# Performance work log

Measured on AMD Instinct MI355X. Metric: run time of the kernel, lower is better.

The kernel has to match this reference:

```python
import math
import jax, jax.numpy as jnp
import numpy as np

B, T, IN, D, H, L = 128, 1024, 32, 128, 8, 2
U = max(1, min(int(5 * math.log(T + 1)), T))  # ProbSparse sampled queries = 34


def setup_inputs() -> dict:
    key = jax.random.key(0)
    ks = jax.random.split(key, 12)
    def w(k, shape):
        fan_in = shape[-2]
        return jax.random.normal(k, shape, jnp.float32) / jnp.sqrt(jnp.float32(fan_in))
    idx = jnp.stack([jax.random.permutation(jax.random.fold_in(ks[1], l), T)[:U]
                     for l in range(L)]).astype(jnp.int64 if jax.config.jax_enable_x64 else jnp.int32)
    return {
        "x": jax.random.normal(ks[0], (B, T, IN), jnp.float32),
        "idx": idx,
        "proj_w": w(ks[2], (IN, D)), "proj_b": jnp.zeros((D,), jnp.float32),
        "wq": w(ks[3], (L, D, D)), "wk": w(ks[4], (L, D, D)), "wv": w(ks[5], (L, D, D)),
        "wo": w(ks[6], (L, D, D)), "wo_b": jnp.zeros((L, D), jnp.float32),
        "ln1_g": jnp.ones((L, D), jnp.float32), "ln1_b": jnp.zeros((L, D), jnp.float32),
        "ff1_w": w(ks[7], (L, D, 4 * D)), "ff1_b": jnp.zeros((L, 4 * D), jnp.float32),
        "ff2_w": w(ks[8], (L, 4 * D, D)), "ff2_b": jnp.zeros((L, D), jnp.float32),
        "ln2_g": jnp.ones((L, D), jnp.float32), "ln2_b": jnp.zeros((L, D), jnp.float32),
        "head_g": jnp.ones((D,), jnp.float32), "head_bb": jnp.zeros((D,), jnp.float32),
        "head_w": w(ks[9], (D, 1)), "head_wb": jnp.zeros((1,), jnp.float32),
    }


def _ln(x, g, b, eps=1e-5):
    m = x.mean(-1, keepdims=True)
    v = ((x - m) ** 2).mean(-1, keepdims=True)
    return (x - m) / jnp.sqrt(v + eps) * g + b


def _pos_encoding():
    pos = jnp.arange(T, dtype=jnp.float32)[:, None]
    div = jnp.exp(jnp.arange(0, D, 2, dtype=jnp.float32) * (-math.log(10000.0) / D))
    # interleave sin/cos -> [T, D]
    return jnp.stack([jnp.sin(pos * div), jnp.cos(pos * div)], axis=-1).reshape(T, D)


def reference(x, idx, proj_w, proj_b, wq, wk, wv, wo, wo_b, ln1_g, ln1_b,
              ff1_w, ff1_b, ff2_w, ff2_b, ln2_g, ln2_b,
              head_g, head_bb, head_w, head_wb):
    Dh = D // H
    h = x @ proj_w + proj_b + _pos_encoding()[None]  # [B,T,D]
    for l in range(L):
        q = (h @ wq[l]).reshape(B, T, H, Dh).transpose(0, 2, 1, 3)
        k = (h @ wk[l]).reshape(B, T, H, Dh).transpose(0, 2, 1, 3)
        v = (h @ wv[l]).reshape(B, T, H, Dh).transpose(0, 2, 1, 3)
        qs = q[:, :, idx[l], :]  # gather sampled queries [B,H,U,Dh]
        scores = jnp.einsum('bhud,bhtd->bhut', qs, k) / jnp.sqrt(jnp.float32(Dh))
        attn = jax.nn.softmax(scores, axis=-1)
        ctx = jnp.einsum('bhut,bhtd->bhud', attn, v)  # [B,H,U,Dh]
        base = jnp.broadcast_to(ctx.mean(axis=2, keepdims=True), (B, H, T, Dh))
        out = base.at[:, :, idx[l], :].set(ctx)  # scatter back
        attn_out = out.transpose(0, 2, 1, 3).reshape(B, T, D) @ wo[l] + wo_b[l]
        h = _ln(h + attn_out, ln1_g[l], ln1_b[l])
        ff = jax.nn.gelu(h @ ff1_w[l] + ff1_b[l], approximate=False) @ ff2_w[l] + ff2_b[l]
        h = _ln(h + ff, ln2_g[l], ln2_b[l])
    last = _ln(h[:, -1, :], head_g, head_bb)
    return (last @ head_w + head_wb).squeeze(-1)  # [B]
```

## Files before the change

kernel.cpp:

```cpp
#include <hip/hip_runtime.h>
#include <math.h>

constexpr int B  = 128;
constexpr int T  = 1024;
constexpr int IN_DIM = 32;
constexpr int D  = 128;
constexpr int H  = 8;
constexpr int DH = 16;
constexpr int L  = 2;
constexpr int U  = 34;
constexpr int FF = 512;

typedef __attribute__((ext_vector_type(8))) _Float16 f16x8;
typedef __attribute__((ext_vector_type(2))) _Float16 h2;
typedef __attribute__((ext_vector_type(4))) float f32x4;

__device__ __forceinline__ unsigned short f2h(float x) {
  union { _Float16 h; unsigned short u; } v;
  v.h = (_Float16)x;
  return v.u;
}

__device__ __forceinline__ h2 shfl_xor_h2(h2 v, int off) {
  union { h2 h; int i; } u;
  u.h = v;
  u.i = __shfl_xor(u.i, off);
  return u.h;
}

__device__ __forceinline__ float erf_fast(float x) {
  float a = fabsf(x);
  float t = __builtin_amdgcn_rcpf(fmaf(0.3275911f, a, 1.f));
  float y = t * (0.254829592f +
            t * (-0.284496736f +
            t * (1.421413741f +
            t * (-1.453152027f +
            t * 1.061405429f))));
  float r = 1.f - y * __expf(-a * a);
  return copysignf(r, x);
}


__device__ __forceinline__ void blockMax2(float& a, float& b, float* red) {
  for (int off = 32; off; off >>= 1) {
    a = fmaxf(a, __shfl_down(a, off));
    b = fmaxf(b, __shfl_down(b, off));
  }
  if ((threadIdx.x & 63) == 0) {
    red[threadIdx.x >> 6] = a;
    red[4 + (threadIdx.x >> 6)] = b;
  }
  __syncthreads();
  a = fmaxf(fmaxf(red[0], red[1]), fmaxf(red[2], red[3]));
  b = fmaxf(fmaxf(red[4], red[5]), fmaxf(red[6], red[7]));
  __syncthreads();
}

__device__ __forceinline__ void blockSum2(float& a, float& b, float* red) {
  for (int off = 32; off; off >>= 1) {
    a += __shfl_down(a, off);
    b += __shfl_down(b, off);
  }
  if ((threadIdx.x & 63) == 0) {
    red[threadIdx.x >> 6] = a;
    red[4 + (threadIdx.x >> 6)] = b;
  }
  __syncthreads();
  a = red[0] + red[1] + red[2] + red[3];
  b = red[4] + red[5] + red[6] + red[7];
  __syncthreads();
}


__global__ void k_prep_all(const float* __restrict__ wk_l,
                           const float* __restrict__ wv_l,
                           const float* __restrict__ w1_l,
                           const float* __restrict__ w2_l,
                           unsigned short* __restrict__ wkT,
                           unsigned short* __restrict__ wvT,
                           unsigned short* __restrict__ w1T,
                           unsigned short* __restrict__ w2T) {
  int idx = blockIdx.x * 256 + threadIdx.x;
  if (idx < 16384) {
    int n = idx >> 7, k = idx & 127;
    wkT[idx] = f2h(wk_l[k * 128 + n]);
  } else if (idx < 32768) {
    int j = idx - 16384;
    int n = j >> 7, k = j & 127;
    wvT[j] = f2h(wv_l[k * 128 + n]);
  } else if (idx < 98304) {
    int j = idx - 32768;
    int n = j >> 7, k = j & 127;
    w1T[j] = f2h(w1_l[k * 512 + n]);
  } else if (idx < 163840) {
    int j = idx - 98304;
    int n = j >> 9, k = j & 511;
    w2T[j] = f2h(w2_l[k * 128 + n]);
  }
}

__global__ __launch_bounds__(D) void k_proj(const float* __restrict__ x,
                                            const float* __restrict__ pw,
                                            const float* __restrict__ pb,
                                            float* __restrict__ h) {
  int row = blockIdx.x;
  int t = row & (T - 1);
  int d = threadIdx.x;
  __shared__ float xs[IN_DIM];
  if (threadIdx.x < IN_DIM) xs[threadIdx.x] = x[(size_t)row * IN_DIM + threadIdx.x];
  __syncthreads();
  float acc = pb[d];
#pragma unroll
  for (int i = 0; i < IN_DIM; ++i) acc += xs[i] * pw[i * D + d];
  int j = d >> 1;
  float div = __expf((float)(2 * j) * (-logf(10000.f) / (float)D));
  float ang = (float)t * div;
  acc += (d & 1) ? __cosf(ang) : __sinf(ang);
  h[(size_t)row * D + d] = acc;
}

__global__ __launch_bounds__(256) void k_kv_mfma2(
    const float* __restrict__ h,
    const unsigned short* __restrict__ wkt,
    const unsigned short* __restrict__ wvt,
    unsigned short* __restrict__ kbuf, unsigned short* __restrict__ vbuf) {
  __shared__ unsigned short hsb[16 * 128];
  const int tid = threadIdx.x;
  const int r0 = blockIdx.x * 16;
  {
    int m = tid >> 4, kc = tid & 15;
    const float* src = h + (size_t)(r0 + m) * D + kc * 8;
    float4 x0 = *(const float4*)src;
    float4 x1 = *(const float4*)(src + 4);
    f16x8 p;
    p[0] = (_Float16)x0.x; p[1] = (_Float16)x0.y;
    p[2] = (_Float16)x0.z; p[3] = (_Float16)x0.w;
    p[4] = (_Float16)x1.x; p[5] = (_Float16)x1.y;
    p[6] = (_Float16)x1.z; p[7] = (_Float16)x1.w;
    int byte = (m << 8) + (kc << 4);
    byte ^= (m & 7) << 4;
    *(f16x8*)((char*)hsb + byte) = p;
  }
  __syncthreads();
  const int wv = tid >> 6;
  const int l15 = tid & 15;
  const int lq = (tid & 63) >> 4;
  f16x8 afr[4];
#pragma unroll
  for (int ks = 0; ks < 4; ++ks) {
    int byte = (l15 << 8) + ks * 64 + (lq << 4);
    byte ^= (l15 & 7) << 4;
    afr[ks] = *(const f16x8*)((const char*)hsb + byte);
  }
  const unsigned short* wt = (wv < 2) ? wkt : wvt;
  unsigned short* outp = (wv < 2) ? kbuf : vbuf;
  const int cw = (wv & 1) * 64;
  f32x4 acc[4];
#pragma unroll
  for (int nt = 0; nt < 4; ++nt) acc[nt] = (f32x4){0.f, 0.f, 0.f, 0.f};
#pragma unroll
  for (int nt = 0; nt < 4; ++nt) {
    const unsigned short* wp = wt + (size_t)(cw + nt * 16 + l15) * 128 + lq * 8;
#pragma unroll
    for (int ks = 0; ks < 4; ++ks) {
      f16x8 bf = *(const f16x8*)(wp + ks * 32);
      acc[nt] = __builtin_amdgcn_mfma_f32_16x16x32_f16(afr[ks], bf, acc[nt], 0, 0, 0);
    }
  }
#pragma unroll
  for (int nt = 0; nt < 4; ++nt) {
    int col = cw + nt * 16 + l15;
    int hcol = col >> 4, dh = col & 15;
#pragma unroll
    for (int r = 0; r < 4; ++r) {
      int row = r0 + 4 * lq + r;
      int b = row >> 10, t = row & (T - 1);
      outp[(((size_t)b * H + hcol) * T + t) * DH + dh] = f2h(acc[nt][r]);
    }
  }
}

__global__ __launch_bounds__(D) void k_qrow(const float* __restrict__ h,
                                            const int* __restrict__ idx,
                                            const float* __restrict__ wq,
                                            float* __restrict__ qs) {
  int bu = blockIdx.x;
  int b = bu / U, u = bu - b * U;
  int t = idx[u];
  __shared__ float hs[D];
  hs[threadIdx.x] = h[((size_t)b * T + t) * D + threadIdx.x];
  __syncthreads();
  int d = threadIdx.x;
  float acc = 0.f;
  for (int k = 0; k < D; ++k) acc += hs[k] * wq[k * D + d];
  qs[(size_t)bu * D + d] = acc;
}

__global__ __launch_bounds__(256) void k_attn6(const float* __restrict__ qs,
                                               const unsigned short* __restrict__ kbuf,
                                               const unsigned short* __restrict__ vbuf,
                                               float* __restrict__ ctx) {
  constexpr int NWG = B * H * 17;
  int bid = blockIdx.x;
  int orig = (bid & 7) * (NWG / 8) + (bid >> 3);
  int up = orig % 17;
  int gb = orig / 17;
  int hh = gb & 7, b = gb >> 3;
  int u0 = up * 2;

  __shared__ float sc[2][T];
  __shared__ h2 qh[2][8];
  __shared__ float red[8];
  __shared__ float redw[4][2][DH];
  const int tid = threadIdx.x;

  if (tid < 16) {
    int uu = tid >> 3, jj = tid & 7;
    const float* qp = qs + ((size_t)b * U + u0 + uu) * D + hh * DH + jj * 2;
    qh[uu][jj] = (h2){(_Float16)qp[0], (_Float16)qp[1]};
  }
  __syncthreads();
  const unsigned short* kg = kbuf + (size_t)gb * T * DH;
  const unsigned short* vg = vbuf + (size_t)gb * T * DH;

  h2 q0[8], q1[8];
#pragma unroll
  for (int j = 0; j < 8; ++j) { q0[j] = qh[0][j]; q1[j] = qh[1][j]; }

  float lmax0 = -1e30f, lmax1 = -1e30f;
  for (int t = tid; t < T; t += 256) {
    const h2* k2 = (const h2*)(kg + t * DH);
    float s0 = 0.f, s1 = 0.f;
#pragma unroll
    for (int j = 0; j < 8; ++j) {
      h2 kv = k2[j];
      s0 = __builtin_amdgcn_fdot2(q0[j], kv, s0, false);
      s1 = __builtin_amdgcn_fdot2(q1[j], kv, s1, false);
    }
    s0 *= 0.25f; s1 *= 0.25f;
    sc[0][t] = s0; sc[1][t] = s1;
    lmax0 = fmaxf(lmax0, s0);
    lmax1 = fmaxf(lmax1, s1);
  }
  blockMax2(lmax0, lmax1, red);
  float lsum0 = 0.f, lsum1 = 0.f;
  for (int t = tid; t < T; t += 256) {
    float e0 = __expf(sc[0][t] - lmax0);
    float e1 = __expf(sc[1][t] - lmax1);
    sc[0][t] = e0; sc[1][t] = e1;
    lsum0 += e0; lsum1 += e1;
  }
  blockSum2(lsum0, lsum1, red);
  float inv0 = 1.f / lsum0;
  float inv1 = 1.f / lsum1;

  h2 p0[8], p1[8];
#pragma unroll
  for (int j = 0; j < 8; ++j) { p0[j] = (h2){0, 0}; p1[j] = (h2){0, 0}; }
  for (int t = tid; t < T; t += 256) {
    const h2* v2 = (const h2*)(vg + t * DH);
    _Float16 a0 = (_Float16)sc[0][t], a1 = (_Float16)sc[1][t];
    h2 a0h = (h2){a0, a0}, a1h = (h2){a1, a1};
#pragma unroll
    for (int j = 0; j < 8; ++j) {
      h2 vv = v2[j];
      p0[j] += a0h * vv;
      p1[j] += a1h * vv;
    }
  }
#pragma unroll
  for (int j = 0; j < 8; ++j) {
#pragma unroll
    for (int off = 32; off; off >>= 1) {
      p0[j] += shfl_xor_h2(p0[j], off);
      p1[j] += shfl_xor_h2(p1[j], off);
    }
  }
  const int wv = tid >> 6, lane = tid & 63;
  if (lane == 0) {
#pragma unroll
    for (int j = 0; j < 8; ++j) {
      redw[wv][0][2 * j]     = (float)p0[j][0];
      redw[wv][0][2 * j + 1] = (float)p0[j][1];
      redw[wv][1][2 * j]     = (float)p1[j][0];
      redw[wv][1][2 * j + 1] = (float)p1[j][1];
    }
  }
  __syncthreads();
  if (tid < 32) {
    int uu = tid >> 4, dh = tid & 15;
    float tot = redw[0][uu][dh] + redw[1][uu][dh] + redw[2][uu][dh] + redw[3][uu][dh];
    float inv = uu ? inv1 : inv0;
    ctx[((size_t)b * U + u0 + uu) * D + hh * DH + dh] = tot * inv;
  }
}

__global__ __launch_bounds__(D) void k_bc(const float* __restrict__ ctx,
                                          const float* __restrict__ wo,
                                          const float* __restrict__ wob,
                                          float* __restrict__ ctxo,
                                          float* __restrict__ baseo) {
  int i = blockIdx.x;
  int b = i / (U + 1), u = i - b * (U + 1);
  int d = threadIdx.x;
  __shared__ float cs[D];
  if (u < U) {
    cs[d] = ctx[((size_t)b * U + u) * D + d];
  } else {
    float s = 0.f;
    for (int uu = 0; uu < U; ++uu) s += ctx[((size_t)b * U + uu) * D + d];
    cs[d] = s * (1.f / (float)U);
  }
  __syncthreads();
  float acc = wob[d];
  for (int k = 0; k < D; ++k) acc += cs[k] * wo[k * D + d];
  if (u < U) ctxo[((size_t)b * U + u) * D + d] = acc;
  else       baseo[(size_t)b * D + d] = acc;
}

__global__ void k_map(const int* __restrict__ idx, int* __restrict__ map) {
  int t = blockIdx.x * 256 + threadIdx.x;
  if (t >= T) return;
  int m = -1;
  for (int u = 0; u < U; ++u)
    if (idx[u] == t) m = u;
  map[t] = m;
}

constexpr int RF2 = 32;
constexpr int YSS = 129;
__global__ __launch_bounds__(512) void k_ff5b(
    const float* __restrict__ h,
    const float* __restrict__ ctxo,
    const float* __restrict__ baseo,
    const int* __restrict__ map,
    const float* __restrict__ g1,
    const float* __restrict__ b1n,
    const unsigned short* __restrict__ w1t,
    const float* __restrict__ b1,
    const unsigned short* __restrict__ w2t,
    const float* __restrict__ b2,
    const float* __restrict__ g2,
    const float* __restrict__ bb2,
    float* __restrict__ hout) {
  __shared__ unsigned short hsb[RF2 * 128];
  __shared__ unsigned short g16[RF2][520];

  const int tid = threadIdx.x;
  const int r0 = blockIdx.x * RF2;

  {
    int m = tid >> 4, kc = tid & 15;
    int row = r0 + m;
    int b = row >> 10, t = row & (T - 1);
    int u = map[t];
    const float* src = (u >= 0) ? ctxo + ((size_t)b * U + u) * D
                                : baseo + (size_t)b * D;
    const float* hp = h + (size_t)row * D + kc * 8;
    float4 x0 = *(const float4*)hp;
    float4 x1 = *(const float4*)(hp + 4);
    float4 a0 = *(const float4*)(src + kc * 8);
    float4 a1 = *(const float4*)(src + kc * 8 + 4);
    float y0 = x0.x + a0.x, y1 = x0.y + a0.y, y2 = x0.z + a0.z, y3 = x0.w + a0.w;
    float y4 = x1.x + a1.x, y5 = x1.y + a1.y, y6 = x1.z + a1.z, y7 = x1.w + a1.w;
    float s = y0 + y1 + y2 + y3 + y4 + y5 + y6 + y7;
#pragma unroll
    for (int off = 8; off; off >>= 1) s += __shfl_xor(s, off, 16);
    float mu = s * (1.f / D);
    float e0 = y0 - mu, e1 = y1 - mu, e2 = y2 - mu, e3 = y3 - mu;
    float e4 = y4 - mu, e5 = y5 - mu, e6 = y6 - mu, e7 = y7 - mu;
    float v2 = e0 * e0 + e1 * e1 + e2 * e2 + e3 * e3 +
               e4 * e4 + e5 * e5 + e6 * e6 + e7 * e7;
#pragma unroll
    for (int off = 8; off; off >>= 1) v2 += __shfl_xor(v2, off, 16);
    float inv = rsqrtf(v2 * (1.f / D) + 1e-5f);
    float4 gv0 = *(const float4*)(g1 + kc * 8);
    float4 gv1 = *(const float4*)(g1 + kc * 8 + 4);
    float4 bv0 = *(const float4*)(b1n + kc * 8);
    float4 bv1 = *(const float4*)(b1n + kc * 8 + 4);
    f16x8 p;
    p[0] = (_Float16)(e0 * inv * gv0.x + bv0.x);
    p[1] = (_Float16)(e1 * inv * gv0.y + bv0.y);
    p[2] = (_Float16)(e2 * inv * gv0.z + bv0.z);
    p[3] = (_Float16)(e3 * inv * gv0.w + bv0.w);
    p[4] = (_Float16)(e4 * inv * gv1.x + bv1.x);
    p[5] = (_Float16)(e5 * inv * gv1.y + bv1.y);
    p[6] = (_Float16)(e6 * inv * gv1.z + bv1.z);
    p[7] = (_Float16)(e7 * inv * gv1.w + bv1.w);
    int byte = (m << 8) + (kc << 4);
    byte ^= (m & 7) << 4;
    *(f16x8*)((char*)hsb + byte) = p;
  }
  __syncthreads();

  const int wv = tid >> 6;
  const int l15 = tid & 15;
  const int lq = (tid & 63) >> 4;

  f16x8 afr[2][4];
#pragma unroll
  for (int mt = 0; mt < 2; ++mt)
#pragma unroll
    for (int ks = 0; ks < 4; ++ks) {
      int m = mt * 16 + l15;
      int byte = (m << 8) + ks * 64 + (lq << 4);
      byte ^= (m & 7) << 4;
      afr[mt][ks] = *(const f16x8*)((const char*)hsb + byte);
    }

  for (int nt = 0; nt < 4; ++nt) {
    int n0 = wv * 64 + nt * 16;
    const unsigned short* wp = w1t + (size_t)(n0 + l15) * 128 + lq * 8;
    f32x4 a0 = (f32x4){0.f, 0.f, 0.f, 0.f};
    f32x4 a1 = (f32x4){0.f, 0.f, 0.f, 0.f};
#pragma unroll
    for (int ks = 0; ks < 4; ++ks) {
      f16x8 bf = *(const f16x8*)(wp + ks * 32);
      a0 = __builtin_amdgcn_mfma_f32_16x16x32_f16(afr[0][ks], bf, a0, 0, 0, 0);
      a1 = __builtin_amdgcn_mfma_f32_16x16x32_f16(afr[1][ks], bf, a1, 0, 0, 0);
    }
    float bcol = b1[n0 + l15];
#pragma unroll
    for (int r = 0; r < 4; ++r) {
      int row0 = 4 * lq + r;
      float v0 = a0[r] + bcol;
      v0 = 0.5f * v0 * (1.f + erf_fast(v0 * 0.70710678118654752f));
      g16[row0][n0 + l15] = f2h(v0);
      float v1 = a1[r] + bcol;
      v1 = 0.5f * v1 * (1.f + erf_fast(v1 * 0.70710678118654752f));
      g16[row0 + 16][n0 + l15] = f2h(v1);
    }
  }
  __syncthreads();

  f32x4 a2a[2], a2b[2];
  a2a[0] = (f32x4){0.f, 0.f, 0.f, 0.f};
  a2a[1] = (f32x4){0.f, 0.f, 0.f, 0.f};
  a2b[0] = (f32x4){0.f, 0.f, 0.f, 0.f};
  a2b[1] = (f32x4){0.f, 0.f, 0.f, 0.f};
  const int ncol = wv * 16 + l15;
  const unsigned short* wp2b = w2t + (size_t)ncol * 512;
  for (int ks = 0; ks < 8; ++ks) {
    int k0 = ks * 32 + lq * 8;
    int k1 = (ks + 8) * 32 + lq * 8;
    f16x8 x0 = *(const f16x8*)&g16[l15][k0];
    f16x8 x1 = *(const f16x8*)&g16[16 + l15][k0];
    f16x8 w0 = *(const f16x8*)(wp2b + k0);
    a2a[0] = __builtin_amdgcn_mfma_f32_16x16x32_f16(x0, w0, a2a[0], 0, 0, 0);
    a2a[1] = __builtin_amdgcn_mfma_f32_16x16x32_f16(x1, w0, a2a[1], 0, 0, 0);
    f16x8 y0 = *(const f16x8*)&g16[l15][k1];
    f16x8 y1 = *(const f16x8*)&g16[16 + l15][k1];
    f16x8 w1 = *(const f16x8*)(wp2b + k1);
    a2b[0] = __builtin_amdgcn_mfma_f32_16x16x32_f16(y0, w1, a2b[0], 0, 0, 0);
    a2b[1] = __builtin_amdgcn_mfma_f32_16x16x32_f16(y1, w1, a2b[1], 0, 0, 0);
  }
  f32x4 acc2[2];
#pragma unroll
  for (int mt = 0; mt < 2; ++mt) {
    acc2[mt][0] = a2a[mt][0] + a2b[mt][0];
    acc2[mt][1] = a2a[mt][1] + a2b[mt][1];
    acc2[mt][2] = a2a[mt][2] + a2b[mt][2];
    acc2[mt][3] = a2a[mt][3] + a2b[mt][3];
  }
  __syncthreads();

  float* ys = (float*)&g16[0][0];
  {
    float bc = b2[ncol];
#pragma unroll
    for (int mt = 0; mt < 2; ++mt)
#pragma unroll
      for (int r = 0; r < 4; ++r) {
        int row = mt * 16 + 4 * lq + r;
        int byte = (row << 8) + ((ncol * 2) ^ ((row & 7) << 4));
        float h1 = (float)(*(const _Float16*)((const char*)hsb + byte));
        ys[row * YSS + ncol] = h1 + acc2[mt][r] + bc;
      }
  }
  __syncthreads();

  {
    int row = tid >> 4, lane16 = tid & 15;
    const float* yr = ys + row * YSS;
    float yv[8];
    float s = 0.f;
#pragma unroll
    for (int j = 0; j < 8; ++j) {
      yv[j] = yr[lane16 + j * 16];
      s += yv[j];
    }
#pragma unroll
    for (int off = 8; off; off >>= 1) s += __shfl_xor(s, off, 16);
    float mu = s * (1.f / D);
    float v2 = 0.f;
#pragma unroll
    for (int j = 0; j < 8; ++j) {
      float e = yv[j] - mu;
      v2 += e * e;
    }
#pragma unroll
    for (int off = 8; off; off >>= 1) v2 += __shfl_xor(v2, off, 16);
    float inv = rsqrtf(v2 * (1.f / D) + 1e-5f);
    float* op = hout + (size_t)(r0 + row) * D;
#pragma unroll
    for (int j = 0; j < 8; ++j) {
      int dd = lane16 + j * 16;
      op[dd] = (yv[j] - mu) * inv * g2[dd] + bb2[dd];
    }
  }
}

__global__ __launch_bounds__(D) void k_head(const float* __restrict__ h,
                                            const float* __restrict__ g,
                                            const float* __restrict__ bb,
                                            const float* __restrict__ hw,
                                            const float* __restrict__ hwb,
                                            float* __restrict__ out) {
  int b = blockIdx.x, d = threadIdx.x;
  float y = h[((size_t)b * T + (T - 1)) * D + d];
  __shared__ float red[2];
  float s = y;
  for (int off = 32; off; off >>= 1) s += __shfl_down(s, off);
  if ((threadIdx.x & 63) == 0) red[threadIdx.x >> 6] = s;
  __syncthreads();
  float m = (red[0] + red[1]) * (1.f / D);
  __syncthreads();
  float e = y - m;
  float v = e * e;
  for (int off = 32; off; off >>= 1) v += __shfl_down(v, off);
  if ((threadIdx.x & 63) == 0) red[threadIdx.x >> 6] = v;
  __syncthreads();
  float inv = rsqrtf((red[0] + red[1]) * (1.f / D) + 1e-5f);
  __syncthreads();
  float last = e * inv * g[d] + bb[d];
  float p = last * hw[d];
  for (int off = 32; off; off >>= 1) p += __shfl_down(p, off);
  if ((threadIdx.x & 63) == 0) red[threadIdx.x >> 6] = p;
  __syncthreads();
  if (threadIdx.x == 0) out[b] = red[0] + red[1] + hwb[0];
}


extern "C" void kernel_launch(void* const* d_in, const int* in_sizes, int n_in,
                              void* d_out, int out_size, void* d_ws, size_t ws_size,
                              hipStream_t stream) {
  const float* x       = (const float*)d_in[0];
  const int*   idx     = (const int*)d_in[1];
  const float* proj_w  = (const float*)d_in[2];
  const float* proj_b  = (const float*)d_in[3];
  const float* wq      = (const float*)d_in[4];
  const float* wk      = (const float*)d_in[5];
  const float* wv      = (const float*)d_in[6];
  const float* wo      = (const float*)d_in[7];
  const float* wo_b    = (const float*)d_in[8];
  const float* ln1_g   = (const float*)d_in[9];
  const float* ln1_b   = (const float*)d_in[10];
  const float* ff1_w   = (const float*)d_in[11];
  const float* ff1_b   = (const float*)d_in[12];
  const float* ff2_w   = (const float*)d_in[13];
  const float* ff2_b   = (const float*)d_in[14];
  const float* ln2_g   = (const float*)d_in[15];
  const float* ln2_b   = (const float*)d_in[16];
  const float* head_g  = (const float*)d_in[17];
  const float* head_bb = (const float*)d_in[18];
  const float* head_w  = (const float*)d_in[19];
  const float* head_wb = (const float*)d_in[20];
  float* out = (float*)d_out;

  float* wsf  = (float*)d_ws;
  float* h    = wsf;
  float* kreg = h    + (size_t)B * T * D;
  float* vreg = kreg + (size_t)B * T * D;
  float* qs   = vreg + (size_t)B * T * D;
  float* ctx  = qs   + (size_t)B * U * D;
  float* ctxo = ctx  + (size_t)B * U * D;
  float* baseo= ctxo + (size_t)B * U * D;
  int*   map  = (int*)(baseo + (size_t)B * D);
  unsigned short* kbuf16 = (unsigned short*)kreg;
  unsigned short* vbuf16 = (unsigned short*)vreg;
  unsigned short* wbuf = (unsigned short*)(map + 1024);
  const size_t PL = 16384 + 16384 + 65536 + 65536;

  for (int l = 0; l < L; ++l) {
    unsigned short* wkT = wbuf + (size_t)l * PL;
    unsigned short* wvT = wkT + 16384;
    unsigned short* w1T = wvT + 16384;
    unsigned short* w2T = w1T + 65536;
    k_prep_all<<<640, 256, 0, stream>>>(wk + (size_t)l * D * D,
                                        wv + (size_t)l * D * D,
                                        ff1_w + (size_t)l * D * FF,
                                        ff2_w + (size_t)l * FF * D,
                                        wkT, wvT, w1T, w2T);
  }

  k_proj<<<B * T, D, 0, stream>>>(x, proj_w, proj_b, h);

  for (int l = 0; l < L; ++l) {
    const float* wq_l = wq + (size_t)l * D * D;
    const float* wo_l = wo + (size_t)l * D * D;
    const int*   idx_l = idx + l * U;
    unsigned short* wkT = wbuf + (size_t)l * PL;
    unsigned short* wvT = wkT + 16384;
    unsigned short* w1T = wvT + 16384;
    unsigned short* w2T = w1T + 65536;

    k_kv_mfma2<<<B * T / 16, 256, 0, stream>>>(h, wkT, wvT, kbuf16, vbuf16);
    k_qrow<<<B * U, D, 0, stream>>>(h, idx_l, wq_l, qs);
    k_attn6<<<B * H * 17, 256, 0, stream>>>(qs, kbuf16, vbuf16, ctx);
    k_bc<<<B * (U + 1), D, 0, stream>>>(ctx, wo_l, wo_b + l * D, ctxo, baseo);
    k_map<<<(T + 255) / 256, 256, 0, stream>>>(idx_l, map);
    k_ff5b<<<B * T / RF2, 512, 0, stream>>>(h, ctxo, baseo, map,
                                            ln1_g + l * D, ln1_b + l * D,
                                            w1T, ff1_b + l * FF,
                                            w2T, ff2_b + l * D,
                                            ln2_g + l * D, ln2_b + l * D, h);
  }

  k_head<<<B, D, 0, stream>>>(h, head_g, head_bb, head_w, head_wb, out);
}
```

Baseline: 765.3 us.

## Restructure FFN kernel so each wave owns 16 rows with streamed FF chunks

The fused LN1+FFN+LN2 kernel is reorganised so each wave independently processes 16 rows. The 512-wide hidden dimension is streamed in 32-column chunks: each chunk's GELU output goes to a tiny per-wave LDS buffer and is immediately consumed by the second GEMM, with accumulators held in registers. All block-level __syncthreads are removed and LN2 is done with in-register shuffles. The intent is to cut block synchronisation and LDS round-trips. In exchange each wave now streams all of W1 and W2 from global/L2 for only 16 rows, so per-row weight traffic goes up, and register pressure rises.

```diff
diff --git a/kernel.cpp b/kernel.cpp
--- a/kernel.cpp
+++ b/kernel.cpp
@@ -327,9 +327,7 @@
   map[t] = m;
 }
 
-constexpr int RF2 = 32;
-constexpr int YSS = 129;
-__global__ __launch_bounds__(512) void k_ff5b(
+__global__ __launch_bounds__(512) void k_ff7(
     const float* __restrict__ h,
     const float* __restrict__ ctxo,
     const float* __restrict__ baseo,
@@ -343,169 +341,155 @@
     const float* __restrict__ g2,
     const float* __restrict__ bb2,
     float* __restrict__ hout) {
-  __shared__ unsigned short hsb[RF2 * 128];
-  __shared__ unsigned short g16[RF2][520];
+  __shared__ __align__(16) char smem[8 * 4096 + 8 * 1280];
 
   const int tid = threadIdx.x;
-  const int r0 = blockIdx.x * RF2;
+  const int w = tid >> 6;
+  const int lane = tid & 63;
+  const int l15 = lane & 15;
+  const int lq = lane >> 4;
+  const int r0 = blockIdx.x * 128 + w * 16;
+  char* h1w = smem + w * 4096;
+  char* gp  = smem + 8 * 4096 + w * 1280;
 
   {
-    int m = tid >> 4, kc = tid & 15;
-    int row = r0 + m;
-    int b = row >> 10, t = row & (T - 1);
-    int u = map[t];
-    const float* src = (u >= 0) ? ctxo + ((size_t)b * U + u) * D
-                                : baseo + (size_t)b * D;
-    const float* hp = h + (size_t)row * D + kc * 8;
-    float4 x0 = *(const float4*)hp;
-    float4 x1 = *(const float4*)(hp + 4);
-    float4 a0 = *(const float4*)(src + kc * 8);
-    float4 a1 = *(const float4*)(src + kc * 8 + 4);
-    float y0 = x0.x + a0.x, y1 = x0.y + a0.y, y2 = x0.z + a0.z, y3 = x0.w + a0.w;
-    float y4 = x1.x + a1.x, y5 = x1.y + a1.y, y6 = x1.z + a1.z, y7 = x1.w + a1.w;
-    float s = y0 + y1 + y2 + y3 + y4 + y5 + y6 + y7;
-#pragma unroll
-    for (int off = 8; off; off >>= 1) s += __shfl_xor(s, off, 16);
-    float mu = s * (1.f / D);
-    float e0 = y0 - mu, e1 = y1 - mu, e2 = y2 - mu, e3 = y3 - mu;
-    float e4 = y4 - mu, e5 = y5 - mu, e6 = y6 - mu, e7 = y7 - mu;
-    float v2 = e0 * e0 + e1 * e1 + e2 * e2 + e3 * e3 +
-               e4 * e4 + e5 * e5 + e6 * e6 + e7 * e7;
-#pragma unroll
-    for (int off = 8; off; off >>= 1) v2 += __shfl_xor(v2, off, 16);
-    float inv = rsqrtf(v2 * (1.f / D) + 1e-5f);
-    float4 gv0 = *(const float4*)(g1 + kc * 8);
-    float4 gv1 = *(const float4*)(g1 + kc * 8 + 4);
-    float4 bv0 = *(const float4*)(b1n + kc * 8);
-    float4 bv1 = *(const float4*)(b1n + kc * 8 + 4);
-    f16x8 p;
-    p[0] = (_Float16)(e0 * inv * gv0.x + bv0.x);
-    p[1] = (_Float16)(e1 * inv * gv0.y + bv0.y);
-    p[2] = (_Float16)(e2 * inv * gv0.z + bv0.z);
-    p[3] = (_Float16)(e3 * inv * gv0.w + bv0.w);
-    p[4] = (_Float16)(e4 * inv * gv1.x + bv1.x);
-    p[5] = (_Float16)(e5 * inv * gv1.y + bv1.y);
-    p[6] = (_Float16)(e6 * inv * gv1.z + bv1.z);
-    p[7] = (_Float16)(e7 * inv * gv1.w + bv1.w);
-    int byte = (m << 8) + (kc << 4);
-    byte ^= (m & 7) << 4;
-    *(f16x8*)((char*)hsb + byte) = p;
-  }
-  __syncthreads();
-
-  const int wv = tid >> 6;
-  const int l15 = tid & 15;
-  const int lq = (tid & 63) >> 4;
-
-  f16x8 afr[2][4];
-#pragma unroll
-  for (int mt = 0; mt < 2; ++mt)
-#pragma unroll
-    for (int ks = 0; ks < 4; ++ks) {
-      int m = mt * 16 + l15;
-      int byte = (m << 8) + ks * 64 + (lq << 4);
-      byte ^= (m & 7) << 4;
-      afr[mt][ks] = *(const f16x8*)((const char*)hsb + byte);
-    }
-
-  for (int nt = 0; nt < 4; ++nt) {
-    int n0 = wv * 64 + nt * 16;
-    const unsigned short* wp = w1t + (size_t)(n0 + l15) * 128 + lq * 8;
-    f32x4 a0 = (f32x4){0.f, 0.f, 0.f, 0.f};
-    f32x4 a1 = (f32x4){0.f, 0.f, 0.f, 0.f};
-#pragma unroll
-    for (int ks = 0; ks < 4; ++ks) {
-      f16x8 bf = *(const f16x8*)(wp + ks * 32);
-      a0 = __builtin_amdgcn_mfma_f32_16x16x32_f16(afr[0][ks], bf, a0, 0, 0, 0);
-      a1 = __builtin_amdgcn_mfma_f32_16x16x32_f16(afr[1][ks], bf, a1, 0, 0, 0);
-    }
-    float bcol = b1[n0 + l15];
-#pragma unroll
-    for (int r = 0; r < 4; ++r) {
-      int row0 = 4 * lq + r;
-      float v0 = a0[r] + bcol;
-      v0 = 0.5f * v0 * (1.f + erf_fast(v0 * 0.70710678118654752f));
-      g16[row0][n0 + l15] = f2h(v0);
-      float v1 = a1[r] + bcol;
-      v1 = 0.5f * v1 * (1.f + erf_fast(v1 * 0.70710678118654752f));
-      g16[row0 + 16][n0 + l15] = f2h(v1);
-    }
-  }
-  __syncthreads();
-
-  f32x4 a2a[2], a2b[2];
-  a2a[0] = (f32x4){0.f, 0.f, 0.f, 0.f};
-  a2a[1] = (f32x4){0.f, 0.f, 0.f, 0.f};
-  a2b[0] = (f32x4){0.f, 0.f, 0.f, 0.f};
-  a2b[1] = (f32x4){0.f, 0.f, 0.f, 0.f};
-  const int ncol = wv * 16 + l15;
-  const unsigned short* wp2b = w2t + (size_t)ncol * 512;
-  for (int ks = 0; ks < 8; ++ks) {
-    int k0 = ks * 32 + lq * 8;
-    int k1 = (ks + 8) * 32 + lq * 8;
-    f16x8 x0 = *(const f16x8*)&g16[l15][k0];
-    f16x8 x1 = *(const f16x8*)&g16[16 + l15][k0];
-    f16x8 w0 = *(const f16x8*)(wp2b + k0);
-    a2a[0] = __builtin_amdgcn_mfma_f32_16x16x32_f16(x0, w0, a2a[0], 0, 0, 0);
-    a2a[1] = __builtin_amdgcn_mfma_f32_16x16x32_f16(x1, w0, a2a[1], 0, 0, 0);
-    f16x8 y0 = *(const f16x8*)&g16[l15][k1];
-    f16x8 y1 = *(const f16x8*)&g16[16 + l15][k1];
-    f16x8 w1 = *(const f16x8*)(wp2b + k1);
-    a2b[0] = __builtin_amdgcn_mfma_f32_16x16x32_f16(y0, w1, a2b[0], 0, 0, 0);
-    a2b[1] = __builtin_amdgcn_mfma_f32_16x16x32_f16(y1, w1, a2b[1], 0, 0, 0);
-  }
-  f32x4 acc2[2];
-#pragma unroll
-  for (int mt = 0; mt < 2; ++mt) {
-    acc2[mt][0] = a2a[mt][0] + a2b[mt][0];
-    acc2[mt][1] = a2a[mt][1] + a2b[mt][1];
-    acc2[mt][2] = a2a[mt][2] + a2b[mt][2];
-    acc2[mt][3] = a2a[mt][3] + a2b[mt][3];
-  }
-  __syncthreads();
-
-  float* ys = (float*)&g16[0][0];
-  {
-    float bc = b2[ncol];
-#pragma unroll
-    for (int mt = 0; mt < 2; ++mt)
-#pragma unroll
-      for (int r = 0; r < 4; ++r) {
-        int row = mt * 16 + 4 * lq + r;
-        int byte = (row << 8) + ((ncol * 2) ^ ((row & 7) << 4));
-        float h1 = (float)(*(const _Float16*)((const char*)hsb + byte));
-        ys[row * YSS + ncol] = h1 + acc2[mt][r] + bc;
-      }
-  }
-  __syncthreads();
-
-  {
-    int row = tid >> 4, lane16 = tid & 15;
-    const float* yr = ys + row * YSS;
-    float yv[8];
+    int row = r0 + l15;
+    int bb = row >> 10, tt = row & (T - 1);
+    int u = map[tt];
+    const float* src = (u >= 0) ? ctxo + ((size_t)bb * U + u) * D
+                                : baseo + (size_t)bb * D;
+    const float* hp = h + (size_t)row * D + lq * 32;
+    const float* ap = src + lq * 32;
+    float y[32];
     float s = 0.f;
 #pragma unroll
     for (int j = 0; j < 8; ++j) {
-      yv[j] = yr[lane16 + j * 16];
-      s += yv[j];
-    }
-#pragma unroll
-    for (int off = 8; off; off >>= 1) s += __shfl_xor(s, off, 16);
+      float4 hv = *(const float4*)(hp + j * 4);
+      float4 av = *(const float4*)(ap + j * 4);
+      y[j * 4 + 0] = hv.x + av.x;
+      y[j * 4 + 1] = hv.y + av.y;
+      y[j * 4 + 2] = hv.z + av.z;
+      y[j * 4 + 3] = hv.w + av.w;
+      s += y[j * 4 + 0] + y[j * 4 + 1] + y[j * 4 + 2] + y[j * 4 + 3];
+    }
+    s += __shfl_xor(s, 16);
+    s += __shfl_xor(s, 32);
     float mu = s * (1.f / D);
     float v2 = 0.f;
 #pragma unroll
-    for (int j = 0; j < 8; ++j) {
-      float e = yv[j] - mu;
+    for (int j = 0; j < 32; ++j) {
+      float e = y[j] - mu;
       v2 += e * e;
     }
-#pragma unroll
-    for (int off = 8; off; off >>= 1) v2 += __shfl_xor(v2, off, 16);
+    v2 += __shfl_xor(v2, 16);
+    v2 += __shfl_xor(v2, 32);
     float inv = rsqrtf(v2 * (1.f / D) + 1e-5f);
-    float* op = hout + (size_t)(r0 + row) * D;
-#pragma unroll
-    for (int j = 0; j < 8; ++j) {
-      int dd = lane16 + j * 16;
-      op[dd] = (yv[j] - mu) * inv * g2[dd] + bb2[dd];
+#pragma unroll
+    for (int c = 0; c < 4; ++c) {
+      int col0 = lq * 32 + c * 8;
+      float4 gv0 = *(const float4*)(g1 + col0);
+      float4 gv1 = *(const float4*)(g1 + col0 + 4);
+      float4 bv0 = *(const float4*)(b1n + col0);
+      float4 bv1 = *(const float4*)(b1n + col0 + 4);
+      f16x8 p;
+      p[0] = (_Float16)((y[c * 8 + 0] - mu) * inv * gv0.x + bv0.x);
+      p[1] = (_Float16)((y[c * 8 + 1] - mu) * inv * gv0.y + bv0.y);
+      p[2] = (_Float16)((y[c * 8 + 2] - mu) * inv * gv0.z + bv0.z);
+      p[3] = (_Float16)((y[c * 8 + 3] - mu) * inv * gv0.w + bv0.w);
+      p[4] = (_Float16)((y[c * 8 + 4] - mu) * inv * gv1.x + bv1.x);
+      p[5] = (_Float16)((y[c * 8 + 5] - mu) * inv * gv1.y + bv1.y);
+      p[6] = (_Float16)((y[c * 8 + 6] - mu) * inv * gv1.z + bv1.z);
+      p[7] = (_Float16)((y[c * 8 + 7] - mu) * inv * gv1.w + bv1.w);
+      int byte = l15 * 256 + col0 * 2;
+      byte ^= (l15 & 7) << 4;
+      *(f16x8*)(h1w + byte) = p;
+    }
+  }
+
+  f16x8 afr[4];
+#pragma unroll
+  for (int ks = 0; ks < 4; ++ks) {
+    int byte = l15 * 256 + ks * 64 + lq * 16;
+    byte ^= (l15 & 7) << 4;
+    afr[ks] = *(const f16x8*)(h1w + byte);
+  }
+
+  f32x4 acc2[8];
+#pragma unroll
+  for (int i = 0; i < 8; ++i) acc2[i] = (f32x4){0.f, 0.f, 0.f, 0.f};
+
+  for (int kt = 0; kt < 16; ++kt) {
+#pragma unroll
+    for (int p = 0; p < 2; ++p) {
+      int n0 = (kt * 2 + p) * 16;
+      const unsigned short* wp = w1t + (size_t)(n0 + l15) * 128 + lq * 8;
+      f32x4 a1 = (f32x4){0.f, 0.f, 0.f, 0.f};
+#pragma unroll
+      for (int ks = 0; ks < 4; ++ks) {
+        f16x8 bf = *(const f16x8*)(wp + ks * 32);
+        a1 = __builtin_amdgcn_mfma_f32_16x16x32_f16(afr[ks], bf, a1, 0, 0, 0);
+      }
+      float bcol = b1[n0 + l15];
+#pragma unroll
+      for (int rr = 0; rr < 4; ++rr) {
+        float v = a1[rr] + bcol;
+        v = 0.5f * v * (1.f + erf_fast(v * 0.70710678118654752f));
+        int byte = (4 * lq + rr) * 80 + (l15 + 16 * p) * 2;
+        *(unsigned short*)(gp + byte) = f2h(v);
+      }
+    }
+    f16x8 a = *(const f16x8*)(gp + l15 * 80 + lq * 16);
+    const unsigned short* wp2 = w2t + (size_t)l15 * 512 + kt * 32 + lq * 8;
+#pragma unroll
+    for (int c2 = 0; c2 < 8; ++c2) {
+      f16x8 bf = *(const f16x8*)(wp2 + (size_t)c2 * 16 * 512);
+      acc2[c2] = __builtin_amdgcn_mfma_f32_16x16x32_f16(a, bf, acc2[c2], 0, 0, 0);
+    }
+  }
+
+#pragma unroll
+  for (int c2 = 0; c2 < 8; ++c2) {
+    int col = c2 * 16 + l15;
+    float bc = b2[col];
+#pragma unroll
+    for (int rr = 0; rr < 4; ++rr) {
+      int lrow = 4 * lq + rr;
+      int byte = lrow * 256 + ((col * 2) ^ ((lrow & 7) << 4));
+      float h1v = (float)(*(const _Float16*)(h1w + byte));
+      acc2[c2][rr] = h1v + acc2[c2][rr] + bc;
+    }
+  }
+  float mu[4], iv[4];
+#pragma unroll
+  for (int rr = 0; rr < 4; ++rr) {
+    float s = 0.f;
+#pragma unroll
+    for (int c2 = 0; c2 < 8; ++c2) s += acc2[c2][rr];
+    s += __shfl_xor(s, 1);
+    s += __shfl_xor(s, 2);
+    s += __shfl_xor(s, 4);
+    s += __shfl_xor(s, 8);
+    mu[rr] = s * (1.f / D);
+    float v2 = 0.f;
+#pragma unroll
+    for (int c2 = 0; c2 < 8; ++c2) {
+      float e = acc2[c2][rr] - mu[rr];
+      v2 += e * e;
+    }
+    v2 += __shfl_xor(v2, 1);
+    v2 += __shfl_xor(v2, 2);
+    v2 += __shfl_xor(v2, 4);
+    v2 += __shfl_xor(v2, 8);
+    iv[rr] = rsqrtf(v2 * (1.f / D) + 1e-5f);
+  }
+#pragma unroll
+  for (int c2 = 0; c2 < 8; ++c2) {
+    int col = c2 * 16 + l15;
+    float gv = g2[col], bv = bb2[col];
+#pragma unroll
+    for (int rr = 0; rr < 4; ++rr) {
+      hout[(size_t)(r0 + 4 * lq + rr) * D + col] =
+          (acc2[c2][rr] - mu[rr]) * iv[rr] * gv + bv;
     }
   }
 }
@@ -609,11 +593,11 @@
     k_attn6<<<B * H * 17, 256, 0, stream>>>(qs, kbuf16, vbuf16, ctx);
     k_bc<<<B * (U + 1), D, 0, stream>>>(ctx, wo_l, wo_b + l * D, ctxo, baseo);
     k_map<<<(T + 255) / 256, 256, 0, stream>>>(idx_l, map);
-    k_ff5b<<<B * T / RF2, 512, 0, stream>>>(h, ctxo, baseo, map,
-                                            ln1_g + l * D, ln1_b + l * D,
-                                            w1T, ff1_b + l * FF,
-                                            w2T, ff2_b + l * D,
-                                            ln2_g + l * D, ln2_b + l * D, h);
+    k_ff7<<<B * T / 128, 512, 0, stream>>>(h, ctxo, baseo, map,
+                                           ln1_g + l * D, ln1_b + l * D,
+                                           w1T, ff1_b + l * FF,
+                                           w2T, ff2_b + l * D,
+                                           ln2_g + l * D, ln2_b + l * D, h);
   }
 
   k_head<<<B, D, 0, stream>>>(h, head_g, head_bb, head_w, head_wb, out);
```

Result: slower. 989.1 us (+29.3%).

## Process four sampled queries per attention block and fold map kernel into bc

Applied to the files above, without the earlier changes.

The attention kernel now handles four sampled queries per workgroup instead of two. Each K/V row loaded from global memory is reused across more queries, and the grid shrinks from 17 to 9 query groups per (batch, head); the last group pads with a clamped query and skips the extra write. The separate idx-to-map kernel is merged into the output-projection kernel as 8 extra blocks, removing one launch per layer. The cost is more registers and shared memory per attention block, which may lower occupancy, plus a small amount of wasted padded work.

```diff
diff --git a/kernel.cpp b/kernel.cpp
--- a/kernel.cpp
+++ b/kernel.cpp
@@ -41,33 +41,36 @@
 }
 
 
-__device__ __forceinline__ void blockMax2(float& a, float& b, float* red) {
-  for (int off = 32; off; off >>= 1) {
-    a = fmaxf(a, __shfl_down(a, off));
-    b = fmaxf(b, __shfl_down(b, off));
-  }
+__device__ __forceinline__ void blockMax4(float* v, float* red) {
+  for (int off = 32; off; off >>= 1)
+#pragma unroll
+    for (int i = 0; i < 4; ++i) v[i] = fmaxf(v[i], __shfl_down(v[i], off));
   if ((threadIdx.x & 63) == 0) {
-    red[threadIdx.x >> 6] = a;
-    red[4 + (threadIdx.x >> 6)] = b;
-  }
-  __syncthreads();
-  a = fmaxf(fmaxf(red[0], red[1]), fmaxf(red[2], red[3]));
-  b = fmaxf(fmaxf(red[4], red[5]), fmaxf(red[6], red[7]));
-  __syncthreads();
-}
-
-__device__ __forceinline__ void blockSum2(float& a, float& b, float* red) {
-  for (int off = 32; off; off >>= 1) {
-    a += __shfl_down(a, off);
-    b += __shfl_down(b, off);
-  }
+    int w = threadIdx.x >> 6;
+#pragma unroll
+    for (int i = 0; i < 4; ++i) red[i * 4 + w] = v[i];
+  }
+  __syncthreads();
+#pragma unroll
+  for (int i = 0; i < 4; ++i)
+    v[i] = fmaxf(fmaxf(red[i * 4], red[i * 4 + 1]),
+                 fmaxf(red[i * 4 + 2], red[i * 4 + 3]));
+  __syncthreads();
+}
+
+__device__ __forceinline__ void blockSum4(float* v, float* red) {
+  for (int off = 32; off; off >>= 1)
+#pragma unroll
+    for (int i = 0; i < 4; ++i) v[i] += __shfl_down(v[i], off);
   if ((threadIdx.x & 63) == 0) {
-    red[threadIdx.x >> 6] = a;
-    red[4 + (threadIdx.x >> 6)] = b;
-  }
-  __syncthreads();
-  a = red[0] + red[1] + red[2] + red[3];
-  b = red[4] + red[5] + red[6] + red[7];
+    int w = threadIdx.x >> 6;
+#pragma unroll
+    for (int i = 0; i < 4; ++i) red[i * 4 + w] = v[i];
+  }
+  __syncthreads();
+#pragma unroll
+  for (int i = 0; i < 4; ++i)
+    v[i] = red[i * 4] + red[i * 4 + 1] + red[i * 4 + 2] + red[i * 4 + 3];
   __syncthreads();
 }
 
@@ -196,111 +199,138 @@
   qs[(size_t)bu * D + d] = acc;
 }
 
-__global__ __launch_bounds__(256) void k_attn6(const float* __restrict__ qs,
+__global__ __launch_bounds__(256) void k_attn7(const float* __restrict__ qs,
                                                const unsigned short* __restrict__ kbuf,
                                                const unsigned short* __restrict__ vbuf,
                                                float* __restrict__ ctx) {
-  constexpr int NWG = B * H * 17;
+  constexpr int UP = 9;
+  constexpr int NWG = B * H * UP;
   int bid = blockIdx.x;
   int orig = (bid & 7) * (NWG / 8) + (bid >> 3);
-  int up = orig % 17;
-  int gb = orig / 17;
+  int up = orig % UP;
+  int gb = orig / UP;
   int hh = gb & 7, b = gb >> 3;
-  int u0 = up * 2;
-
-  __shared__ float sc[2][T];
-  __shared__ h2 qh[2][8];
-  __shared__ float red[8];
-  __shared__ float redw[4][2][DH];
+  int u0 = up * 4;
+
+  __shared__ float sc[4][T];
+  __shared__ h2 qh[4][8];
+  __shared__ float red[16];
+  __shared__ float redw[4][4][DH];
   const int tid = threadIdx.x;
 
-  if (tid < 16) {
+  if (tid < 32) {
     int uu = tid >> 3, jj = tid & 7;
-    const float* qp = qs + ((size_t)b * U + u0 + uu) * D + hh * DH + jj * 2;
+    int us = u0 + uu; if (us >= U) us = U - 1;
+    const float* qp = qs + ((size_t)b * U + us) * D + hh * DH + jj * 2;
     qh[uu][jj] = (h2){(_Float16)qp[0], (_Float16)qp[1]};
   }
   __syncthreads();
   const unsigned short* kg = kbuf + (size_t)gb * T * DH;
   const unsigned short* vg = vbuf + (size_t)gb * T * DH;
 
-  h2 q0[8], q1[8];
-#pragma unroll
-  for (int j = 0; j < 8; ++j) { q0[j] = qh[0][j]; q1[j] = qh[1][j]; }
-
-  float lmax0 = -1e30f, lmax1 = -1e30f;
+  h2 q[4][8];
+#pragma unroll
+  for (int u = 0; u < 4; ++u)
+#pragma unroll
+    for (int j = 0; j < 8; ++j) q[u][j] = qh[u][j];
+
+  float lmax[4] = {-1e30f, -1e30f, -1e30f, -1e30f};
   for (int t = tid; t < T; t += 256) {
     const h2* k2 = (const h2*)(kg + t * DH);
-    float s0 = 0.f, s1 = 0.f;
+    float s[4] = {0.f, 0.f, 0.f, 0.f};
 #pragma unroll
     for (int j = 0; j < 8; ++j) {
       h2 kv = k2[j];
-      s0 = __builtin_amdgcn_fdot2(q0[j], kv, s0, false);
-      s1 = __builtin_amdgcn_fdot2(q1[j], kv, s1, false);
-    }
-    s0 *= 0.25f; s1 *= 0.25f;
-    sc[0][t] = s0; sc[1][t] = s1;
-    lmax0 = fmaxf(lmax0, s0);
-    lmax1 = fmaxf(lmax1, s1);
-  }
-  blockMax2(lmax0, lmax1, red);
-  float lsum0 = 0.f, lsum1 = 0.f;
+#pragma unroll
+      for (int u = 0; u < 4; ++u)
+        s[u] = __builtin_amdgcn_fdot2(q[u][j], kv, s[u], false);
+    }
+#pragma unroll
+    for (int u = 0; u < 4; ++u) {
+      s[u] *= 0.25f;
+      sc[u][t] = s[u];
+      lmax[u] = fmaxf(lmax[u], s[u]);
+    }
+  }
+  blockMax4(lmax, red);
+  float lsum[4] = {0.f, 0.f, 0.f, 0.f};
   for (int t = tid; t < T; t += 256) {
-    float e0 = __expf(sc[0][t] - lmax0);
-    float e1 = __expf(sc[1][t] - lmax1);
-    sc[0][t] = e0; sc[1][t] = e1;
-    lsum0 += e0; lsum1 += e1;
-  }
-  blockSum2(lsum0, lsum1, red);
-  float inv0 = 1.f / lsum0;
-  float inv1 = 1.f / lsum1;
-
-  h2 p0[8], p1[8];
-#pragma unroll
-  for (int j = 0; j < 8; ++j) { p0[j] = (h2){0, 0}; p1[j] = (h2){0, 0}; }
+#pragma unroll
+    for (int u = 0; u < 4; ++u) {
+      float e = __expf(sc[u][t] - lmax[u]);
+      sc[u][t] = e;
+      lsum[u] += e;
+    }
+  }
+  blockSum4(lsum, red);
+  float inv[4];
+#pragma unroll
+  for (int u = 0; u < 4; ++u) inv[u] = 1.f / lsum[u];
+
+  h2 p[4][8];
+#pragma unroll
+  for (int u = 0; u < 4; ++u)
+#pragma unroll
+    for (int j = 0; j < 8; ++j) p[u][j] = (h2){0, 0};
   for (int t = tid; t < T; t += 256) {
     const h2* v2 = (const h2*)(vg + t * DH);
-    _Float16 a0 = (_Float16)sc[0][t], a1 = (_Float16)sc[1][t];
-    h2 a0h = (h2){a0, a0}, a1h = (h2){a1, a1};
+    h2 ah[4];
+#pragma unroll
+    for (int u = 0; u < 4; ++u) {
+      _Float16 a = (_Float16)sc[u][t];
+      ah[u] = (h2){a, a};
+    }
 #pragma unroll
     for (int j = 0; j < 8; ++j) {
       h2 vv = v2[j];
-      p0[j] += a0h * vv;
-      p1[j] += a1h * vv;
-    }
-  }
-#pragma unroll
-  for (int j = 0; j < 8; ++j) {
-#pragma unroll
-    for (int off = 32; off; off >>= 1) {
-      p0[j] += shfl_xor_h2(p0[j], off);
-      p1[j] += shfl_xor_h2(p1[j], off);
-    }
-  }
+#pragma unroll
+      for (int u = 0; u < 4; ++u) p[u][j] += ah[u] * vv;
+    }
+  }
+#pragma unroll
+  for (int u = 0; u < 4; ++u)
+#pragma unroll
+    for (int j = 0; j < 8; ++j)
+#pragma unroll
+      for (int off = 32; off; off >>= 1)
+        p[u][j] += shfl_xor_h2(p[u][j], off);
+
   const int wv = tid >> 6, lane = tid & 63;
   if (lane == 0) {
 #pragma unroll
-    for (int j = 0; j < 8; ++j) {
-      redw[wv][0][2 * j]     = (float)p0[j][0];
-      redw[wv][0][2 * j + 1] = (float)p0[j][1];
-      redw[wv][1][2 * j]     = (float)p1[j][0];
-      redw[wv][1][2 * j + 1] = (float)p1[j][1];
-    }
-  }
-  __syncthreads();
-  if (tid < 32) {
+    for (int u = 0; u < 4; ++u)
+#pragma unroll
+      for (int j = 0; j < 8; ++j) {
+        redw[wv][u][2 * j]     = (float)p[u][j][0];
+        redw[wv][u][2 * j + 1] = (float)p[u][j][1];
+      }
+  }
+  __syncthreads();
+  if (tid < 64) {
     int uu = tid >> 4, dh = tid & 15;
-    float tot = redw[0][uu][dh] + redw[1][uu][dh] + redw[2][uu][dh] + redw[3][uu][dh];
-    float inv = uu ? inv1 : inv0;
-    ctx[((size_t)b * U + u0 + uu) * D + hh * DH + dh] = tot * inv;
-  }
-}
-
-__global__ __launch_bounds__(D) void k_bc(const float* __restrict__ ctx,
-                                          const float* __restrict__ wo,
-                                          const float* __restrict__ wob,
-                                          float* __restrict__ ctxo,
-                                          float* __restrict__ baseo) {
+    if (u0 + uu < U) {
+      float tot = redw[0][uu][dh] + redw[1][uu][dh] + redw[2][uu][dh] + redw[3][uu][dh];
+      ctx[((size_t)b * U + u0 + uu) * D + hh * DH + dh] = tot * inv[uu];
+    }
+  }
+}
+
+__global__ __launch_bounds__(D) void k_bc2(const float* __restrict__ ctx,
+                                           const float* __restrict__ wo,
+                                           const float* __restrict__ wob,
+                                           const int* __restrict__ idx,
+                                           float* __restrict__ ctxo,
+                                           float* __restrict__ baseo,
+                                           int* __restrict__ map) {
   int i = blockIdx.x;
+  if (i >= B * (U + 1)) {
+    int t = (i - B * (U + 1)) * D + threadIdx.x;
+    int m = -1;
+    for (int u = 0; u < U; ++u)
+      if (idx[u] == t) m = u;
+    map[t] = m;
+    return;
+  }
   int b = i / (U + 1), u = i - b * (U + 1);
   int d = threadIdx.x;
   __shared__ float cs[D];
@@ -316,15 +346,6 @@
   for (int k = 0; k < D; ++k) acc += cs[k] * wo[k * D + d];
   if (u < U) ctxo[((size_t)b * U + u) * D + d] = acc;
   else       baseo[(size_t)b * D + d] = acc;
-}
-
-__global__ void k_map(const int* __restrict__ idx, int* __restrict__ map) {
-  int t = blockIdx.x * 256 + threadIdx.x;
-  if (t >= T) return;
-  int m = -1;
-  for (int u = 0; u < U; ++u)
-    if (idx[u] == t) m = u;
-  map[t] = m;
 }
 
 constexpr int RF2 = 32;
@@ -606,9 +627,9 @@
 
     k_kv_mfma2<<<B * T / 16, 256, 0, stream>>>(h, wkT, wvT, kbuf16, vbuf16);
     k_qrow<<<B * U, D, 0, stream>>>(h, idx_l, wq_l, qs);
-    k_attn6<<<B * H * 17, 256, 0, stream>>>(qs, kbuf16, vbuf16, ctx);
-    k_bc<<<B * (U + 1), D, 0, stream>>>(ctx, wo_l, wo_b + l * D, ctxo, baseo);
-    k_map<<<(T + 255) / 256, 256, 0, stream>>>(idx_l, map);
+    k_attn7<<<B * H * 9, 256, 0, stream>>>(qs, kbuf16, vbuf16, ctx);
+    k_bc2<<<B * (U + 1) + 8, D, 0, stream>>>(ctx, wo_l, wo_b + l * D, idx_l,
+                                             ctxo, baseo, map);
     k_ff5b<<<B * T / RF2, 512, 0, stream>>>(h, ctxo, baseo, map,
                                             ln1_g + l * D, ln1_b + l * D,
                                             w1T, ff1_b + l * FF,
```

New measurement: 776.0 us. No clear change (+1.4%).
